# Performance work log

Measured on AMD Instinct MI355X. Metric: run time of the kernel, lower is better.

## Reference

```python
import jax, jax.numpy as jnp
import numpy as np

N_NODES = 65536
N_EDGES = 524288
N_GRAPHS = 512
G_NODES = 10000
NUM_DISEASES = 2000
IN_DIM = 128
HID = 256  # 2 * IN_DIM (z_emb concat feat)
D_FEAT = 512
C_FEAT = 512
MAX_Z = 4000


def setup_inputs() -> dict:
    key = jax.random.key(0)
    ks = jax.random.split(key, 20)
    rn = lambda k, shape: jax.random.normal(k, shape, dtype=jnp.float32) * 0.05
    return {
        "z": jax.random.randint(ks[0], (N_NODES,), 0, MAX_Z),
        "node_id": jnp.sort(jax.random.randint(ks[1], (N_NODES,), 0, G_NODES)),
        "src": jax.random.randint(ks[2], (N_EDGES,), 0, N_NODES),
        "dst": jax.random.randint(ks[3], (N_EDGES,), 0, N_NODES),
        "graph_ids": jnp.sort(jax.random.randint(ks[4], (N_NODES,), 0, N_GRAPHS)),
        "z_table": rn(ks[5], (MAX_Z, IN_DIM)),
        "d_feat_tab": rn(ks[6], (G_NODES, D_FEAT)),
        "c_feat_tab": rn(ks[7], (G_NODES, C_FEAT)),
        "Wd": rn(ks[8], (D_FEAT, IN_DIM)),
        "Wc": rn(ks[9], (C_FEAT, IN_DIM)),
        "gin_W1": rn(ks[10], (HID, HID)), "gin_b1": jnp.zeros((HID,), jnp.float32),
        "gin_W2": rn(ks[11], (HID, HID)), "gin_b2": jnp.zeros((HID,), jnp.float32),
        "sage_Wself": rn(ks[12], (HID, HID)),
        "sage_Wneigh": rn(ks[13], (HID, HID)),
        "sage_b": jnp.zeros((HID,), jnp.float32),
        "lin1_W": rn(ks[14], (HID, HID)), "lin1_b": jnp.zeros((HID,), jnp.float32),
        "lin2_W": rn(ks[15], (HID, 1)), "lin2_b": jnp.zeros((1,), jnp.float32),
    }


def reference(z, node_id, src, dst, graph_ids, z_table, d_feat_tab, c_feat_tab,
              Wd, Wc, gin_W1, gin_b1, gin_W2, gin_b2,
              sage_Wself, sage_Wneigh, sage_b, lin1_W, lin1_b, lin2_W, lin2_b):
    # --- input feature construction (Model.forward) ---
    z_emb = z_table[z]                               # [N, IN_DIM]
    d_proj = d_feat_tab[node_id] @ Wd                # d_fc (bias=False)
    c_proj = c_feat_tab[node_id] @ Wc                # c_fc (bias=False)
    disease = (node_id <= NUM_DISEASES)[:, None]
    # node_id is sorted -> masked concat order == node order
    feat = jnp.where(disease, d_proj, c_proj)        # [N, IN_DIM]
    x = jnp.concatenate([z_emb, feat], axis=1)       # [N, HID]
    # --- GINConv: sum aggregation, eps=0, mlp = Lin->ReLU->Lin ---
    agg = jax.ops.segment_sum(x[src], dst, num_segments=N_NODES)
    h = x + agg
    h = jax.nn.relu(h @ gin_W1 + gin_b1) @ gin_W2 + gin_b2
    # --- SAGEConv('mean'): fc_self(h) + fc_neigh(mean_neighbors) + bias ---
    deg = jax.ops.segment_sum(jnp.ones((N_EDGES,), h.dtype), dst, num_segments=N_NODES)
    mean_n = jax.ops.segment_sum(h[src], dst, num_segments=N_NODES) / jnp.maximum(deg, 1.0)[:, None]
    h = h @ sage_Wself + mean_n @ sage_Wneigh + sage_b
    # --- per-graph max pooling readout ---
    g = jax.ops.segment_max(h, graph_ids, num_segments=N_GRAPHS, indices_are_sorted=True)
    g = jnp.where(jnp.isfinite(g), g, 0.0)           # guard empty graphs
    # --- head: Linear -> ReLU -> (dropout p=0, eval) -> Linear ---
    h = jax.nn.relu(g @ lin1_W + lin1_b)
    return h @ lin2_W + lin2_b                       # [N_GRAPHS, 1]
```

## Files before the change

### kernel.cpp

```cpp
#include <hip/hip_runtime.h>
#include <hip/hip_bf16.h>

#define N_NODES     65536
#define N_EDGES     524288
#define N_GRAPHS    512
#define G_NODES_N   10000
#define NUM_DIS     2000
#define IN_DIM      128
#define HID         256
#define D_FEAT      512
#define MAX_Z       4000

typedef _Float16 half8 __attribute__((ext_vector_type(8)));
typedef float    f32x4 __attribute__((ext_vector_type(4)));

typedef __attribute__((address_space(1))) const void as1_void;
typedef __attribute__((address_space(3))) void       as3_void;

__global__ __launch_bounds__(256) void prep_kernel(
    const float* __restrict__ Ws, const float* __restrict__ Wn,
    const float* __restrict__ Wd, const float* __restrict__ Wc,
    const float* __restrict__ W1, const float* __restrict__ W2,
    const float* __restrict__ z_table,
    const int* __restrict__ z, const int* __restrict__ node_id,
    _Float16* __restrict__ WsT, _Float16* __restrict__ WnT,
    _Float16* __restrict__ WdT, _Float16* __restrict__ WcT,
    _Float16* __restrict__ W12P, _Float16* __restrict__ zt16,
    int2* __restrict__ zn2, int* __restrict__ cnt, int* __restrict__ flags)
{
    const int b = blockIdx.x;
    const int tid = threadIdx.x;
    if (b < 64) {
        __shared__ float tile[64][65];
        const float* W; _Float16* T; int K, N, k0, n0;
        if (b < 32) {
            const int mat = b >> 4, t = b & 15;
            K = HID; N = HID; k0 = (t >> 2) * 64; n0 = (t & 3) * 64;
            W = (mat == 0) ? Ws : Wn;
            T = (mat == 0) ? WsT : WnT;
        } else {
            const int bb = b - 32;
            const int mat = bb >> 4, t = bb & 15;
            K = D_FEAT; N = IN_DIM; k0 = (t >> 1) * 64; n0 = (t & 1) * 64;
            W = (mat == 0) ? Wd : Wc;
            T = (mat == 0) ? WdT : WcT;
        }
        const int tx = tid & 63, ty = tid >> 6;
        #pragma unroll
        for (int r = 0; r < 64; r += 4)
            tile[r + ty][tx] = W[(size_t)(k0 + r + ty) * N + n0 + tx];
        __syncthreads();
        #pragma unroll
        for (int c = 0; c < 64; c += 4)
            T[(size_t)(n0 + c + ty) * K + k0 + tx] = (_Float16)tile[tx][c + ty];
    } else if (b < 576) {
        const int bb = b - 64;
        const int mat = bb >> 8;
        const int k = bb & 255;
        const int n = tid;
        const float* W = mat ? W2 : W1;
        const float v = W[(size_t)k * HID + n];
        const size_t idx = (size_t)(mat * 8 + (k >> 5)) * 8192
                         + (size_t)((((k >> 3) & 3) * 256 + n) * 8 + (k & 7));
        W12P[idx] = (_Float16)v;
    } else if (b < 826) {
        const size_t base = ((size_t)(b - 576) * 256 + tid) * 8;
        const float4 f0 = *(const float4*)(z_table + base);
        const float4 f1 = *(const float4*)(z_table + base + 4);
        half8 h;
        h[0]=(_Float16)f0.x; h[1]=(_Float16)f0.y; h[2]=(_Float16)f0.z; h[3]=(_Float16)f0.w;
        h[4]=(_Float16)f1.x; h[5]=(_Float16)f1.y; h[6]=(_Float16)f1.z; h[7]=(_Float16)f1.w;
        *(half8*)(zt16 + base) = h;
    } else if (b < 890) {
        const int base = (b - 826) * 1024 + tid * 4;
        *(int4*)(cnt + base) = make_int4(0, 0, 0, 0);
        if (b == 826 && tid < 128) flags[tid] = 0;
    } else {
        const int i = (b - 890) * 256 + tid;
        zn2[i] = make_int2(z[i] << 8, node_id[i] << 8);
    }
}

__global__ __launch_bounds__(256) void proj_hist_kernel(
    const float* __restrict__ dtab, const float* __restrict__ ctab,
    const _Float16* __restrict__ WdT, const _Float16* __restrict__ WcT,
    _Float16* __restrict__ proj,
    const int* __restrict__ dst, int* __restrict__ cnt)
{
    const int blk = blockIdx.x;
    if (blk >= 79) {
        const int e = (blk - 79) * 256 + threadIdx.x;
        if (e < N_EDGES) atomicAdd(&cnt[dst[e]], 1);
        return;
    }
    __shared__ _Float16 Alds[128 * 40];
    __shared__ _Float16 Blds[128 * 40];
    const float* tab; const _Float16* WT; int base, M, bm;
    if (blk < 16) { tab = dtab; WT = WdT; base = 0;           M = NUM_DIS + 1;             bm = blk * 128; }
    else          { tab = ctab; WT = WcT; base = NUM_DIS + 1; M = G_NODES_N - NUM_DIS - 1; bm = (blk - 16) * 128; }
    const int tid  = threadIdx.x;
    const int wave = tid >> 6, lane = tid & 63;
    const int q    = lane >> 4, l16 = lane & 15;
    const int mbase = (wave & 1) * 64, nbase = (wave >> 1) * 64;
    const int r = tid >> 1, s = tid & 1;

    f32x4 acc[4][4] = {};

    for (int kc = 0; kc < 16; ++kc) {
        const int k0 = kc * 32;
        const int arow = min(bm + r, M - 1);
        const float* gA = tab + (size_t)(base + arow) * D_FEAT + k0 + s * 16;
        const _Float16* gB = WT + (size_t)r * D_FEAT + k0 + s * 16;
        const float4 f0 = ((const float4*)gA)[0];
        const float4 f1 = ((const float4*)gA)[1];
        const float4 f2 = ((const float4*)gA)[2];
        const float4 f3 = ((const float4*)gA)[3];
        const half8 hb0 = *(const half8*)gB;
        const half8 hb1 = *(const half8*)(gB + 8);
        half8 h0, h1;
        h0[0]=(_Float16)f0.x; h0[1]=(_Float16)f0.y; h0[2]=(_Float16)f0.z; h0[3]=(_Float16)f0.w;
        h0[4]=(_Float16)f1.x; h0[5]=(_Float16)f1.y; h0[6]=(_Float16)f1.z; h0[7]=(_Float16)f1.w;
        h1[0]=(_Float16)f2.x; h1[1]=(_Float16)f2.y; h1[2]=(_Float16)f2.z; h1[3]=(_Float16)f2.w;
        h1[4]=(_Float16)f3.x; h1[5]=(_Float16)f3.y; h1[6]=(_Float16)f3.z; h1[7]=(_Float16)f3.w;
        __syncthreads();
        *(half8*)&Alds[r * 40 + s * 16]     = h0;
        *(half8*)&Alds[r * 40 + s * 16 + 8] = h1;
        *(half8*)&Blds[r * 40 + s * 16]     = hb0;
        *(half8*)&Blds[r * 40 + s * 16 + 8] = hb1;
        __syncthreads();
        half8 a[4], b[4];
        #pragma unroll
        for (int i = 0; i < 4; ++i)
            a[i] = *(const half8*)&Alds[(mbase + i * 16 + l16) * 40 + q * 8];
        #pragma unroll
        for (int j = 0; j < 4; ++j)
            b[j] = *(const half8*)&Blds[(nbase + j * 16 + l16) * 40 + q * 8];
        #pragma unroll
        for (int i = 0; i < 4; ++i)
            #pragma unroll
            for (int j = 0; j < 4; ++j)
                acc[i][j] = __builtin_amdgcn_mfma_f32_16x16x32_f16(a[i], b[j], acc[i][j], 0, 0, 0);
    }

    #pragma unroll
    for (int j = 0; j < 4; ++j) {
        const int colg = nbase + j * 16 + l16;
        #pragma unroll
        for (int i = 0; i < 4; ++i) {
            #pragma unroll
            for (int rr = 0; rr < 4; ++rr) {
                const int row = bm + mbase + i * 16 + q * 4 + rr;
                if (row < M)
                    proj[(size_t)(base + row) * IN_DIM + colg] = (_Float16)acc[i][j][rr];
            }
        }
    }
}

__global__ __launch_bounds__(256) void scan_fused_kernel(
    const int* __restrict__ cnt, int* __restrict__ row_ptr,
    int* __restrict__ fill, int* __restrict__ flags)
{
    __shared__ int a[256], b[256];
    __shared__ int sums[64];
    __shared__ int segbase;
    const int t = threadIdx.x;
    const int blk = blockIdx.x;
    const int base = blk * 1024 + t * 4;
    const int4 c = *(const int4*)(cnt + base);
    const int s = c.x + c.y + c.z + c.w;
    a[t] = s;
    __syncthreads();
    int* in = a; int* out = b;
    for (int off = 1; off < 256; off <<= 1) {
        out[t] = in[t] + ((t >= off) ? in[t - off] : 0);
        __syncthreads();
        int* tmp = in; in = out; out = tmp;
    }
    if (t == 0) {
        atomicExch(&flags[64 + blk], in[255]);
        __threadfence();
        atomicAdd(&flags[0], 1);
        while (atomicAdd(&flags[0], 0) < 64) {}
    }
    __syncthreads();
    if (t < 64) sums[t] = atomicAdd(&flags[64 + t], 0);
    __syncthreads();
    if (t == 0) {
        int pfx = 0;
        for (int i = 0; i < blk; ++i) pfx += sums[i];
        segbase = pfx;
        if (blk == 63) {
            int tot = pfx;
            for (int i = blk; i < 64; ++i) tot += sums[i];
            row_ptr[N_NODES] = tot;
        }
    }
    __syncthreads();
    const int run = in[t] - s + segbase;
    int4 r;
    r.x = run; r.y = run + c.x; r.z = r.y + c.y; r.w = r.z + c.z;
    *(int4*)(row_ptr + base) = r;
    *(int4*)(fill + base) = r;
}

__global__ __launch_bounds__(256) void scatter_kernel(
    const int* __restrict__ src, const int* __restrict__ dst,
    const int2* __restrict__ zn2,
    int* __restrict__ fill, int* __restrict__ col, int2* __restrict__ colzn)
{
    const int e = blockIdx.x * 256 + threadIdx.x;
    if (e < N_EDGES) {
        const int s = src[e];
        const int pos = atomicAdd(&fill[dst[e]], 1);
        col[pos] = s;
        colzn[pos] = zn2[s];
    }
}

__global__ __launch_bounds__(512) void gin_fused_kernel(
    const int* __restrict__ row_ptr, const int2* __restrict__ colzn,
    const int2* __restrict__ zn2,
    const _Float16* __restrict__ zt16, const _Float16* __restrict__ proj,
    const _Float16* __restrict__ W12P,
    const float* __restrict__ b1, const float* __restrict__ b2,
    _Float16* __restrict__ H)
{
    __shared__ _Float16 Apanel[64 * 264];
    __shared__ _Float16 Blds[8192];

    const int bm   = blockIdx.x * 64;
    const int tid  = threadIdx.x;
    const int wave = tid >> 6, lane = tid & 63;
    const int q    = lane >> 4, l16 = lane & 15;
    const int wr   = wave >> 2;
    const int wc   = wave & 3;
    const int rbase = wr * 32;
    const int nbase = wc * 64;

    #pragma unroll
    for (int tt = 0; tt < 2; ++tt) {
        const int seg = (wave * 2 + tt) * 64 + lane;
        __builtin_amdgcn_global_load_lds((as1_void*)(W12P + seg * 8),
            (as3_void*)&Blds[(wave * 2 + tt) * 64 * 8], 16, 0, 0);
    }

    {
        const int p = tid & 7;
        const int r = tid >> 3;
        const int gr = bm + r;
        const int beg = row_ptr[gr], end = row_ptr[gr + 1];
        const char* ztb = (const char*)zt16 + p * 32;
        const char* prb = (const char*)proj + p * 32;
        float za[16], pa[16];
        {
            const int2 zn = zn2[gr];
            const half8* zp = (const half8*)(ztb + zn.x);
            const half8* pp = (const half8*)(prb + zn.y);
            const half8 z0 = zp[0], z1 = zp[1], p0 = pp[0], p1 = pp[1];
            #pragma unroll
            for (int i = 0; i < 8; ++i) {
                za[i] = (float)z0[i]; za[8 + i] = (float)z1[i];
                pa[i] = (float)p0[i]; pa[8 + i] = (float)p1[i];
            }
        }
        int e = beg;
        int2 iA, iB, iC, iD;
        if (e + 4 <= end) {
            iA = colzn[e]; iB = colzn[e + 1]; iC = colzn[e + 2]; iD = colzn[e + 3];
        }
        for (; e + 4 <= end; e += 4) {
            const half8* zpA = (const half8*)(ztb + iA.x);
            const half8* ppA = (const half8*)(prb + iA.y);
            const half8* zpB = (const half8*)(ztb + iB.x);
            const half8* ppB = (const half8*)(prb + iB.y);
            const half8* zpC = (const half8*)(ztb + iC.x);
            const half8* ppC = (const half8*)(prb + iC.y);
            const half8* zpD = (const half8*)(ztb + iD.x);
            const half8* ppD = (const half8*)(prb + iD.y);
            const half8 zA0 = zpA[0], zA1 = zpA[1], pA0 = ppA[0], pA1 = ppA[1];
            const half8 zB0 = zpB[0], zB1 = zpB[1], pB0 = ppB[0], pB1 = ppB[1];
            const half8 zC0 = zpC[0], zC1 = zpC[1], pC0 = ppC[0], pC1 = ppC[1];
            const half8 zD0 = zpD[0], zD1 = zpD[1], pD0 = ppD[0], pD1 = ppD[1];
            if (e + 8 <= end) {
                iA = colzn[e + 4]; iB = colzn[e + 5];
                iC = colzn[e + 6]; iD = colzn[e + 7];
            }
            #pragma unroll
            for (int i = 0; i < 8; ++i) {
                za[i]     += ((float)zA0[i] + (float)zB0[i]) + ((float)zC0[i] + (float)zD0[i]);
                za[8 + i] += ((float)zA1[i] + (float)zB1[i]) + ((float)zC1[i] + (float)zD1[i]);
                pa[i]     += ((float)pA0[i] + (float)pB0[i]) + ((float)pC0[i] + (float)pD0[i]);
                pa[8 + i] += ((float)pA1[i] + (float)pB1[i]) + ((float)pC1[i] + (float)pD1[i]);
            }
        }
        for (; e + 2 <= end; e += 2) {
            const int2 jA = colzn[e];
            const int2 jB = colzn[e + 1];
            const half8* zpA = (const half8*)(ztb + jA.x);
            const half8* ppA = (const half8*)(prb + jA.y);
            const half8* zpB = (const half8*)(ztb + jB.x);
            const half8* ppB = (const half8*)(prb + jB.y);
            const half8 zA0 = zpA[0], zA1 = zpA[1], pA0 = ppA[0], pA1 = ppA[1];
            const half8 zB0 = zpB[0], zB1 = zpB[1], pB0 = ppB[0], pB1 = ppB[1];
            #pragma unroll
            for (int i = 0; i < 8; ++i) {
                za[i]     += (float)zA0[i] + (float)zB0[i];
                za[8 + i] += (float)zA1[i] + (float)zB1[i];
                pa[i]     += (float)pA0[i] + (float)pB0[i];
                pa[8 + i] += (float)pA1[i] + (float)pB1[i];
            }
        }
        if (e < end) {
            const int2 jA = colzn[e];
            const half8* zp = (const half8*)(ztb + jA.x);
            const half8* pp = (const half8*)(prb + jA.y);
            const half8 z0 = zp[0], z1 = zp[1], p0 = pp[0], p1 = pp[1];
            #pragma unroll
            for (int i = 0; i < 8; ++i) {
                za[i] += (float)z0[i]; za[8 + i] += (float)z1[i];
                pa[i] += (float)p0[i]; pa[8 + i] += (float)p1[i];
            }
        }
        half8 oz0, oz1, op0, op1;
        #pragma unroll
        for (int i = 0; i < 8; ++i) {
            oz0[i] = (_Float16)za[i];     oz1[i] = (_Float16)za[8 + i];
            op0[i] = (_Float16)pa[i];     op1[i] = (_Float16)pa[8 + i];
        }
        *(half8*)&Apanel[r * 264 + p * 16]           = oz0;
        *(half8*)&Apanel[r * 264 + p * 16 + 8]       = oz1;
        *(half8*)&Apanel[r * 264 + 128 + p * 16]     = op0;
        *(half8*)&Apanel[r * 264 + 128 + p * 16 + 8] = op1;
    }
    __syncthreads();

    half8 pf0, pf1;
    auto pfetch = [&](int c) {
        const _Float16* s = W12P + (size_t)c * 8192 + (size_t)tid * 8;
        pf0 = *(const half8*)(s);
        pf1 = *(const half8*)(s + 4096);
    };
    pfetch(1);

    f32x4 acc[2][4] = {};
    for (int c = 0; c < 16; ++c) {
        const int kl = (c & 7) * 32;
        half8 a[2], b[4];
        #pragma unroll
        for (int i = 0; i < 2; ++i)
            a[i] = *(const half8*)&Apanel[(rbase + i * 16 + l16) * 264 + kl + q * 8];
        #pragma unroll
        for (int j = 0; j < 4; ++j)
            b[j] = *(const half8*)&Blds[(q * 256 + nbase + j * 16 + l16) * 8];
        #pragma unroll
        for (int i = 0; i < 2; ++i)
            #pragma unroll
            for (int j = 0; j < 4; ++j)
                acc[i][j] = __builtin_amdgcn_mfma_f32_16x16x32_f16(a[i], b[j], acc[i][j], 0, 0, 0);
        if (c == 15) break;
        __syncthreads();
        *(half8*)&Blds[tid * 8]         = pf0;
        *(half8*)&Blds[(tid + 512) * 8] = pf1;
        if (c == 7) {
            #pragma unroll
            for (int j = 0; j < 4; ++j) {
                const int colg = nbase + j * 16 + l16;
                const float bv = b1[colg];
                #pragma unroll
                for (int i = 0; i < 2; ++i)
                    #pragma unroll
                    for (int rr = 0; rr < 4; ++rr) {
                        const float v = fmaxf(acc[i][j][rr] + bv, 0.0f);
                        Apanel[(rbase + i * 16 + q * 4 + rr) * 264 + colg] = (_Float16)v;
                        acc[i][j][rr] = 0.0f;
                    }
            }
        }
        if (c < 14) pfetch(c + 2);
        __syncthreads();
    }

    #pragma unroll
    for (int j = 0; j < 4; ++j) {
        const int colg = nbase + j * 16 + l16;
        const float bv = b2[colg];
        #pragma unroll
        for (int i = 0; i < 2; ++i)
            #pragma unroll
            for (int rr = 0; rr < 4; ++rr) {
                const int rowg = bm + rbase + i * 16 + q * 4 + rr;
                H[(size_t)rowg * HID + colg] = (_Float16)(acc[i][j][rr] + bv);
            }
    }
}

__global__ __launch_bounds__(256) void csr_agg_kernel(
    const int* __restrict__ row_ptr, const int* __restrict__ col,
    const _Float16* __restrict__ F, _Float16* __restrict__ OUT)
{
    const int t = blockIdx.x * 256 + threadIdx.x;
    const int d = t >> 5;
    const int q = t & 31;
    const int beg = row_ptr[d];
    const int end = row_ptr[d + 1];
    float acc[8] = {0.f,0.f,0.f,0.f,0.f,0.f,0.f,0.f};
    int e = beg;
    for (; e + 8 <= end; e += 8) {
        const int s0 = col[e],     s1 = col[e + 1];
        const int s2 = col[e + 2], s3 = col[e + 3];
        const int s4 = col[e + 4], s5 = col[e + 5];
        const int s6 = col[e + 6], s7 = col[e + 7];
        const half8 v0 = *(const half8*)(F + (size_t)s0 * HID + q * 8);
        const half8 v1 = *(const half8*)(F + (size_t)s1 * HID + q * 8);
        const half8 v2 = *(const half8*)(F + (size_t)s2 * HID + q * 8);
        const half8 v3 = *(const half8*)(F + (size_t)s3 * HID + q * 8);
        const half8 v4 = *(const half8*)(F + (size_t)s4 * HID + q * 8);
        const half8 v5 = *(const half8*)(F + (size_t)s5 * HID + q * 8);
        const half8 v6 = *(const half8*)(F + (size_t)s6 * HID + q * 8);
        const half8 v7 = *(const half8*)(F + (size_t)s7 * HID + q * 8);
        #pragma unroll
        for (int i = 0; i < 8; ++i)
            acc[i] += (((float)v0[i] + (float)v1[i]) + ((float)v2[i] + (float)v3[i]))
                    + (((float)v4[i] + (float)v5[i]) + ((float)v6[i] + (float)v7[i]));
    }
    for (; e + 4 <= end; e += 4) {
        const int s0 = col[e],     s1 = col[e + 1];
        const int s2 = col[e + 2], s3 = col[e + 3];
        const half8 v0 = *(const half8*)(F + (size_t)s0 * HID + q * 8);
        const half8 v1 = *(const half8*)(F + (size_t)s1 * HID + q * 8);
        const half8 v2 = *(const half8*)(F + (size_t)s2 * HID + q * 8);
        const half8 v3 = *(const half8*)(F + (size_t)s3 * HID + q * 8);
        #pragma unroll
        for (int i = 0; i < 8; ++i)
            acc[i] += ((float)v0[i] + (float)v1[i]) + ((float)v2[i] + (float)v3[i]);
    }
    for (; e < end; ++e) {
        const half8 v0 = *(const half8*)(F + (size_t)col[e] * HID + q * 8);
        #pragma unroll
        for (int i = 0; i < 8; ++i) acc[i] += (float)v0[i];
    }
    const float rs = 1.0f / fmaxf((float)(end - beg), 1.0f);
    half8 o;
    #pragma unroll
    for (int i = 0; i < 8; ++i) o[i] = (_Float16)(acc[i] * rs);
    *(half8*)(OUT + (size_t)d * HID + q * 8) = o;
}

__global__ __launch_bounds__(256) void mfma_gemm_kernel(
    const _Float16* __restrict__ A1, const _Float16* __restrict__ A2,
    const _Float16* __restrict__ B1T, const _Float16* __restrict__ B2T,
    const float* __restrict__ bias, _Float16* __restrict__ Ch)
{
    __shared__ _Float16 Alds[128 * 32];
    __shared__ _Float16 Blds[128 * 32];
    const int bm   = blockIdx.x * 128;
    const int bn   = blockIdx.y * 128;
    const int tid  = threadIdx.x;
    const int wave = tid >> 6, lane = tid & 63;
    const int q    = lane >> 4, l16 = lane & 15;
    const int mbase = (wave & 1) * 64, nbase = (wave >> 1) * 64;

    const int i0 = wave * 128 + lane;
    const int i1 = i0 + 64;
    const int r0 = i0 >> 2, s0 = i0 & 3;
    const int r1 = i1 >> 2, s1 = i1 & 3;

    half8 pa0, pa1, pb0, pb1;
    auto pfetch = [&](int kc) {
        const int k0 = (kc & 7) * 32;
        const _Float16* Ab = (kc < 8) ? A1 : A2;
        const _Float16* Bb = (kc < 8) ? B1T : B2T;
        pa0 = *(const half8*)(Ab + (size_t)(bm + r0) * HID + k0 + s0 * 8);
        pa1 = *(const half8*)(Ab + (size_t)(bm + r1) * HID + k0 + s1 * 8);
        pb0 = *(const half8*)(Bb + (size_t)(bn + r0) * HID + k0 + s0 * 8);
        pb1 = *(const half8*)(Bb + (size_t)(bn + r1) * HID + k0 + s1 * 8);
    };
    pfetch(0);

    f32x4 acc[4][4] = {};

    for (int kc = 0; kc < 16; ++kc) {
        __syncthreads();
        *(half8*)&Alds[i0 * 8] = pa0;
        *(half8*)&Alds[i1 * 8] = pa1;
        *(half8*)&Blds[i0 * 8] = pb0;
        *(half8*)&Blds[i1 * 8] = pb1;
        if (kc < 15) pfetch(kc + 1);
        __syncthreads();
        half8 a[4], b[4];
        #pragma unroll
        for (int i = 0; i < 4; ++i)
            a[i] = *(const half8*)&Alds[(mbase + i * 16 + l16) * 32 + q * 8];
        #pragma unroll
        for (int j = 0; j < 4; ++j)
            b[j] = *(const half8*)&Blds[(nbase + j * 16 + l16) * 32 + q * 8];
        #pragma unroll
        for (int i = 0; i < 4; ++i)
            #pragma unroll
            for (int j = 0; j < 4; ++j)
                acc[i][j] = __builtin_amdgcn_mfma_f32_16x16x32_f16(a[i], b[j], acc[i][j], 0, 0, 0);
    }

    #pragma unroll
    for (int j = 0; j < 4; ++j) {
        const int colg = bn + nbase + j * 16 + l16;
        const float bv = bias[colg];
        #pragma unroll
        for (int i = 0; i < 4; ++i) {
            #pragma unroll
            for (int rr = 0; rr < 4; ++rr) {
                const int rowg = bm + mbase + i * 16 + q * 4 + rr;
                Ch[(size_t)rowg * HID + colg] = (_Float16)(acc[i][j][rr] + bv);
            }
        }
    }
}

__global__ __launch_bounds__(256) void pool_head_kernel(
    const _Float16* __restrict__ H2, const int* __restrict__ gid,
    const float* __restrict__ W1, const float* __restrict__ b1,
    const float* __restrict__ W2, const float* __restrict__ b2,
    float* __restrict__ out)
{
    const int g = blockIdx.x;
    const int tid = threadIdx.x;
    int lo = 0, hi = N_NODES;
    while (lo < hi) { const int mid = (lo + hi) >> 1; if (gid[mid] < g) lo = mid + 1; else hi = mid; }
    const int start = lo;
    hi = N_NODES;
    while (lo < hi) { const int mid = (lo + hi) >> 1; if (gid[mid] < g + 1) lo = mid + 1; else hi = mid; }
    const int end = lo;

    const int rowofs = tid >> 5;
    const int q = tid & 31;
    float m8[8];
    #pragma unroll
    for (int k = 0; k < 8; ++k) m8[k] = -INFINITY;
    for (int i = start + rowofs; i < end; i += 8) {
        const half8 v = *(const half8*)(H2 + (size_t)i * HID + q * 8);
        #pragma unroll
        for (int k = 0; k < 8; ++k) m8[k] = fmaxf(m8[k], (float)v[k]);
    }
    __shared__ float part[8][256];
    #pragma unroll
    for (int k = 0; k < 8; ++k) part[rowofs][q * 8 + k] = m8[k];
    __syncthreads();
    __shared__ float row[HID];
    __shared__ float red[HID];
    const int j = tid;
    float m = part[0][j];
    #pragma unroll
    for (int r = 1; r < 8; ++r) m = fmaxf(m, part[r][j]);
    row[j] = (m == -INFINITY) ? 0.0f : m;
    __syncthreads();
    float acc = b1[j];
    #pragma unroll 8
    for (int k = 0; k < HID; ++k)
        acc = fmaf(row[k], W1[k * HID + j], acc);
    acc = fmaxf(acc, 0.f);
    red[j] = acc * W2[j];
    __syncthreads();
    for (int s = 128; s > 0; s >>= 1) {
        if (j < s) red[j] += red[j + s];
        __syncthreads();
    }
    if (j == 0) out[g] = red[0] + b2[0];
}

extern "C" void kernel_launch(void* const* d_in, const int* in_sizes, int n_in,
                              void* d_out, int out_size, void* d_ws, size_t ws_size,
                              hipStream_t stream)
{
    const int*   z         = (const int*)d_in[0];
    const int*   node_id   = (const int*)d_in[1];
    const int*   src       = (const int*)d_in[2];
    const int*   dst       = (const int*)d_in[3];
    const int*   graph_ids = (const int*)d_in[4];
    const float* z_table   = (const float*)d_in[5];
    const float* d_feat    = (const float*)d_in[6];
    const float* c_feat    = (const float*)d_in[7];
    const float* Wd        = (const float*)d_in[8];
    const float* Wc        = (const float*)d_in[9];
    const float* gin_W1    = (const float*)d_in[10];
    const float* gin_b1    = (const float*)d_in[11];
    const float* gin_W2    = (const float*)d_in[12];
    const float* gin_b2    = (const float*)d_in[13];
    const float* sage_Wself  = (const float*)d_in[14];
    const float* sage_Wneigh = (const float*)d_in[15];
    const float* sage_b    = (const float*)d_in[16];
    const float* lin1_W    = (const float*)d_in[17];
    const float* lin1_b    = (const float*)d_in[18];
    const float* lin2_W    = (const float*)d_in[19];
    const float* lin2_b    = (const float*)d_in[20];
    float* out = (float*)d_out;

    const size_t NH = (size_t)N_NODES * HID;
    char* wsb = (char*)d_ws;
    _Float16* Hh   = (_Float16*)wsb;                     wsb += NH * 2;
    _Float16* AGGh = (_Float16*)wsb;                     wsb += NH * 2;
    _Float16* H2h  = (_Float16*)wsb;                     wsb += NH * 2;
    _Float16* projh= (_Float16*)wsb;                     wsb += (size_t)G_NODES_N * IN_DIM * 2;
    _Float16* W12P = (_Float16*)wsb;                     wsb += 16 * 8192 * 2;
    _Float16* WsT  = (_Float16*)wsb;                     wsb += HID * HID * 2;
    _Float16* WnT  = (_Float16*)wsb;                     wsb += HID * HID * 2;
    _Float16* WdT  = (_Float16*)wsb;                     wsb += D_FEAT * IN_DIM * 2;
    _Float16* WcT  = (_Float16*)wsb;                     wsb += D_FEAT * IN_DIM * 2;
    _Float16* zt16 = (_Float16*)wsb;                     wsb += (size_t)MAX_Z * IN_DIM * 2;
    int2* zn2      = (int2*)wsb;                         wsb += (size_t)N_NODES * 8;
    int2* colzn    = (int2*)wsb;                         wsb += (size_t)(N_EDGES + 8) * 8;
    int* row_ptr   = (int*)wsb;                          wsb += (N_NODES + 4) * 4;
    int* cnt       = (int*)wsb;                          wsb += N_NODES * 4;
    int* fill      = (int*)wsb;                          wsb += N_NODES * 4;
    int* col       = (int*)wsb;                          wsb += N_EDGES * 4;
    int* flags     = (int*)wsb;                          wsb += 128 * 4;

    prep_kernel<<<1146, 256, 0, stream>>>(
        sage_Wself, sage_Wneigh, Wd, Wc, gin_W1, gin_W2, z_table, z, node_id,
        WsT, WnT, WdT, WcT, W12P, zt16, zn2, cnt, flags);

    proj_hist_kernel<<<79 + N_EDGES / 256, 256, 0, stream>>>(
        d_feat, c_feat, WdT, WcT, projh, dst, cnt);

    scan_fused_kernel<<<64, 256, 0, stream>>>(cnt, row_ptr, fill, flags);
    scatter_kernel<<<N_EDGES / 256, 256, 0, stream>>>(src, dst, zn2, fill, col, colzn);

    gin_fused_kernel<<<N_NODES / 64, 512, 0, stream>>>(
        row_ptr, colzn, zn2, zt16, projh, W12P, gin_b1, gin_b2, Hh);

    csr_agg_kernel<<<(N_NODES * 32) / 256, 256, 0, stream>>>(row_ptr, col, Hh, AGGh);

    dim3 ggrid(N_NODES / 128, HID / 128);
    mfma_gemm_kernel<<<ggrid, 256, 0, stream>>>(Hh, AGGh, WsT, WnT, sage_b, H2h);

    pool_head_kernel<<<N_GRAPHS, 256, 0, stream>>>(
        H2h, graph_ids, lin1_W, lin1_b, lin2_W, lin2_b, out);
}
```

Baseline: 345.4 us.

## Rebalance kernel fusion: histogram into prep, scatter with projection, 256-thread GIN blocks

The edge histogram now runs inside the prep kernel, and zeroing of cnt/flags moves to hipMemsetAsync. The dst-to-CSR scatter now shares a launch with the d/c feature projection GEMM, which removes one launch and overlaps the projection with the atomic scatter. The GIN fused kernel drops from 512 to 256 threads per block, so each wave computes 64 rows x 64 cols and each thread aggregates two node rows sequentially. This lowers per-block parallelism in the gather phase but gives each wave more MFMA reuse.

```diff
diff --git a/kernel.cpp b/kernel.cpp
--- a/kernel.cpp
+++ b/kernel.cpp
@@ -17,16 +17,17 @@
 typedef __attribute__((address_space(1))) const void as1_void;
 typedef __attribute__((address_space(3))) void       as3_void;
 
-__global__ __launch_bounds__(256) void prep_kernel(
+__global__ __launch_bounds__(256) void prep_hist_kernel(
     const float* __restrict__ Ws, const float* __restrict__ Wn,
     const float* __restrict__ Wd, const float* __restrict__ Wc,
     const float* __restrict__ W1, const float* __restrict__ W2,
     const float* __restrict__ z_table,
     const int* __restrict__ z, const int* __restrict__ node_id,
+    const int* __restrict__ dst,
     _Float16* __restrict__ WsT, _Float16* __restrict__ WnT,
     _Float16* __restrict__ WdT, _Float16* __restrict__ WcT,
     _Float16* __restrict__ W12P, _Float16* __restrict__ zt16,
-    int2* __restrict__ zn2, int* __restrict__ cnt, int* __restrict__ flags)
+    int2* __restrict__ zn2, int* __restrict__ cnt)
 {
     const int b = blockIdx.x;
     const int tid = threadIdx.x;
@@ -71,30 +72,83 @@
         h[0]=(_Float16)f0.x; h[1]=(_Float16)f0.y; h[2]=(_Float16)f0.z; h[3]=(_Float16)f0.w;
         h[4]=(_Float16)f1.x; h[5]=(_Float16)f1.y; h[6]=(_Float16)f1.z; h[7]=(_Float16)f1.w;
         *(half8*)(zt16 + base) = h;
-    } else if (b < 890) {
-        const int base = (b - 826) * 1024 + tid * 4;
-        *(int4*)(cnt + base) = make_int4(0, 0, 0, 0);
-        if (b == 826 && tid < 128) flags[tid] = 0;
+    } else if (b < 1082) {
+        const int i = (b - 826) * 256 + tid;
+        zn2[i] = make_int2(z[i] << 8, node_id[i] << 8);
     } else {
-        const int i = (b - 890) * 256 + tid;
-        zn2[i] = make_int2(z[i] << 8, node_id[i] << 8);
-    }
-}
-
-__global__ __launch_bounds__(256) void proj_hist_kernel(
+        const int e = (b - 1082) * 256 + tid;
+        atomicAdd(&cnt[dst[e]], 1);
+    }
+}
+
+__global__ __launch_bounds__(256) void scan_fused_kernel(
+    const int* __restrict__ cnt, int* __restrict__ row_ptr,
+    int* __restrict__ fill, int* __restrict__ flags)
+{
+    __shared__ int a[256], b[256];
+    __shared__ int sums[64];
+    __shared__ int segbase;
+    const int t = threadIdx.x;
+    const int blk = blockIdx.x;
+    const int base = blk * 1024 + t * 4;
+    const int4 c = *(const int4*)(cnt + base);
+    const int s = c.x + c.y + c.z + c.w;
+    a[t] = s;
+    __syncthreads();
+    int* in = a; int* out = b;
+    for (int off = 1; off < 256; off <<= 1) {
+        out[t] = in[t] + ((t >= off) ? in[t - off] : 0);
+        __syncthreads();
+        int* tmp = in; in = out; out = tmp;
+    }
+    if (t == 0) {
+        atomicExch(&flags[64 + blk], in[255]);
+        __threadfence();
+        atomicAdd(&flags[0], 1);
+        while (atomicAdd(&flags[0], 0) < 64) {}
+    }
+    __syncthreads();
+    if (t < 64) sums[t] = atomicAdd(&flags[64 + t], 0);
+    __syncthreads();
+    if (t == 0) {
+        int pfx = 0;
+        for (int i = 0; i < blk; ++i) pfx += sums[i];
+        segbase = pfx;
+        if (blk == 63) {
+            int tot = pfx;
+            for (int i = blk; i < 64; ++i) tot += sums[i];
+            row_ptr[N_NODES] = tot;
+        }
+    }
+    __syncthreads();
+    const int run = in[t] - s + segbase;
+    int4 r;
+    r.x = run; r.y = run + c.x; r.z = r.y + c.y; r.w = r.z + c.z;
+    *(int4*)(row_ptr + base) = r;
+    *(int4*)(fill + base) = r;
+}
+
+__global__ __launch_bounds__(256) void scatter_proj_kernel(
     const float* __restrict__ dtab, const float* __restrict__ ctab,
     const _Float16* __restrict__ WdT, const _Float16* __restrict__ WcT,
     _Float16* __restrict__ proj,
-    const int* __restrict__ dst, int* __restrict__ cnt)
-{
+    const int* __restrict__ src, const int* __restrict__ dst,
+    const int2* __restrict__ zn2,
+    int* __restrict__ fill, int* __restrict__ col, int2* __restrict__ colzn)
+{
+    __shared__ _Float16 Alds[128 * 40];
+    __shared__ _Float16 Blds[128 * 40];
     const int blk = blockIdx.x;
     if (blk >= 79) {
         const int e = (blk - 79) * 256 + threadIdx.x;
-        if (e < N_EDGES) atomicAdd(&cnt[dst[e]], 1);
+        if (e < N_EDGES) {
+            const int s = src[e];
+            const int pos = atomicAdd(&fill[dst[e]], 1);
+            col[pos] = s;
+            colzn[pos] = zn2[s];
+        }
         return;
     }
-    __shared__ _Float16 Alds[128 * 40];
-    __shared__ _Float16 Blds[128 * 40];
     const float* tab; const _Float16* WT; int base, M, bm;
     if (blk < 16) { tab = dtab; WT = WdT; base = 0;           M = NUM_DIS + 1;             bm = blk * 128; }
     else          { tab = ctab; WT = WcT; base = NUM_DIS + 1; M = G_NODES_N - NUM_DIS - 1; bm = (blk - 16) * 128; }
@@ -157,68 +211,7 @@
     }
 }
 
-__global__ __launch_bounds__(256) void scan_fused_kernel(
-    const int* __restrict__ cnt, int* __restrict__ row_ptr,
-    int* __restrict__ fill, int* __restrict__ flags)
-{
-    __shared__ int a[256], b[256];
-    __shared__ int sums[64];
-    __shared__ int segbase;
-    const int t = threadIdx.x;
-    const int blk = blockIdx.x;
-    const int base = blk * 1024 + t * 4;
-    const int4 c = *(const int4*)(cnt + base);
-    const int s = c.x + c.y + c.z + c.w;
-    a[t] = s;
-    __syncthreads();
-    int* in = a; int* out = b;
-    for (int off = 1; off < 256; off <<= 1) {
-        out[t] = in[t] + ((t >= off) ? in[t - off] : 0);
-        __syncthreads();
-        int* tmp = in; in = out; out = tmp;
-    }
-    if (t == 0) {
-        atomicExch(&flags[64 + blk], in[255]);
-        __threadfence();
-        atomicAdd(&flags[0], 1);
-        while (atomicAdd(&flags[0], 0) < 64) {}
-    }
-    __syncthreads();
-    if (t < 64) sums[t] = atomicAdd(&flags[64 + t], 0);
-    __syncthreads();
-    if (t == 0) {
-        int pfx = 0;
-        for (int i = 0; i < blk; ++i) pfx += sums[i];
-        segbase = pfx;
-        if (blk == 63) {
-            int tot = pfx;
-            for (int i = blk; i < 64; ++i) tot += sums[i];
-            row_ptr[N_NODES] = tot;
-        }
-    }
-    __syncthreads();
-    const int run = in[t] - s + segbase;
-    int4 r;
-    r.x = run; r.y = run + c.x; r.z = r.y + c.y; r.w = r.z + c.z;
-    *(int4*)(row_ptr + base) = r;
-    *(int4*)(fill + base) = r;
-}
-
-__global__ __launch_bounds__(256) void scatter_kernel(
-    const int* __restrict__ src, const int* __restrict__ dst,
-    const int2* __restrict__ zn2,
-    int* __restrict__ fill, int* __restrict__ col, int2* __restrict__ colzn)
-{
-    const int e = blockIdx.x * 256 + threadIdx.x;
-    if (e < N_EDGES) {
-        const int s = src[e];
-        const int pos = atomicAdd(&fill[dst[e]], 1);
-        col[pos] = s;
-        colzn[pos] = zn2[s];
-    }
-}
-
-__global__ __launch_bounds__(512) void gin_fused_kernel(
+__global__ __launch_bounds__(256) void gin_fused_kernel(
     const int* __restrict__ row_ptr, const int2* __restrict__ colzn,
     const int2* __restrict__ zn2,
     const _Float16* __restrict__ zt16, const _Float16* __restrict__ proj,
@@ -233,146 +226,151 @@
     const int tid  = threadIdx.x;
     const int wave = tid >> 6, lane = tid & 63;
     const int q    = lane >> 4, l16 = lane & 15;
-    const int wr   = wave >> 2;
-    const int wc   = wave & 3;
-    const int rbase = wr * 32;
-    const int nbase = wc * 64;
-
-    #pragma unroll
-    for (int tt = 0; tt < 2; ++tt) {
-        const int seg = (wave * 2 + tt) * 64 + lane;
+    const int nbase = wave * 64;
+    const int sb   = wave * 256 + lane;
+
+    #pragma unroll
+    for (int tt = 0; tt < 4; ++tt) {
+        const int seg = (wave * 4 + tt) * 64 + lane;
         __builtin_amdgcn_global_load_lds((as1_void*)(W12P + seg * 8),
-            (as3_void*)&Blds[(wave * 2 + tt) * 64 * 8], 16, 0, 0);
+            (as3_void*)&Blds[(wave * 4 + tt) * 64 * 8], 16, 0, 0);
     }
 
     {
         const int p = tid & 7;
-        const int r = tid >> 3;
-        const int gr = bm + r;
-        const int beg = row_ptr[gr], end = row_ptr[gr + 1];
         const char* ztb = (const char*)zt16 + p * 32;
         const char* prb = (const char*)proj + p * 32;
-        float za[16], pa[16];
-        {
-            const int2 zn = zn2[gr];
-            const half8* zp = (const half8*)(ztb + zn.x);
-            const half8* pp = (const half8*)(prb + zn.y);
-            const half8 z0 = zp[0], z1 = zp[1], p0 = pp[0], p1 = pp[1];
+        #pragma unroll 1
+        for (int pass = 0; pass < 2; ++pass) {
+            const int r  = (tid >> 3) + (pass << 5);
+            const int gr = bm + r;
+            const int beg = row_ptr[gr], end = row_ptr[gr + 1];
+            float za[16], pa[16];
+            {
+                const int2 zn = zn2[gr];
+                const half8* zp = (const half8*)(ztb + zn.x);
+                const half8* pp = (const half8*)(prb + zn.y);
+                const half8 z0 = zp[0], z1 = zp[1], p0 = pp[0], p1 = pp[1];
+                #pragma unroll
+                for (int i = 0; i < 8; ++i) {
+                    za[i] = (float)z0[i]; za[8 + i] = (float)z1[i];
+                    pa[i] = (float)p0[i]; pa[8 + i] = (float)p1[i];
+                }
+            }
+            int e = beg;
+            int2 iA, iB, iC, iD;
+            if (e + 4 <= end) {
+                iA = colzn[e]; iB = colzn[e + 1]; iC = colzn[e + 2]; iD = colzn[e + 3];
+            }
+            for (; e + 4 <= end; e += 4) {
+                const half8* zpA = (const half8*)(ztb + iA.x);
+                const half8* ppA = (const half8*)(prb + iA.y);
+                const half8* zpB = (const half8*)(ztb + iB.x);
+                const half8* ppB = (const half8*)(prb + iB.y);
+                const half8* zpC = (const half8*)(ztb + iC.x);
+                const half8* ppC = (const half8*)(prb + iC.y);
+                const half8* zpD = (const half8*)(ztb + iD.x);
+                const half8* ppD = (const half8*)(prb + iD.y);
+                const half8 zA0 = zpA[0], zA1 = zpA[1], pA0 = ppA[0], pA1 = ppA[1];
+                const half8 zB0 = zpB[0], zB1 = zpB[1], pB0 = ppB[0], pB1 = ppB[1];
+                const half8 zC0 = zpC[0], zC1 = zpC[1], pC0 = ppC[0], pC1 = ppC[1];
+                const half8 zD0 = zpD[0], zD1 = zpD[1], pD0 = ppD[0], pD1 = ppD[1];
+                if (e + 8 <= end) {
+                    iA = colzn[e + 4]; iB = colzn[e + 5];
+                    iC = colzn[e + 6]; iD = colzn[e + 7];
+                }
+                #pragma unroll
+                for (int i = 0; i < 8; ++i) {
+                    za[i]     += ((float)zA0[i] + (float)zB0[i]) + ((float)zC0[i] + (float)zD0[i]);
+                    za[8 + i] += ((float)zA1[i] + (float)zB1[i]) + ((float)zC1[i] + (float)zD1[i]);
+                    pa[i]     += ((float)pA0[i] + (float)pB0[i]) + ((float)pC0[i] + (float)pD0[i]);
+                    pa[8 + i] += ((float)pA1[i] + (float)pB1[i]) + ((float)pC1[i] + (float)pD1[i]);
+                }
+            }
+            for (; e + 2 <= end; e += 2) {
+                const int2 jA = colzn[e];
+                const int2 jB = colzn[e + 1];
+                const half8* zpA = (const half8*)(ztb + jA.x);
+                const half8* ppA = (const half8*)(prb + jA.y);
+                const half8* zpB = (const half8*)(ztb + jB.x);
+                const half8* ppB = (const half8*)(prb + jB.y);
+                const half8 zA0 = zpA[0], zA1 = zpA[1], pA0 = ppA[0], pA1 = ppA[1];
+                const half8 zB0 = zpB[0], zB1 = zpB[1], pB0 = ppB[0], pB1 = ppB[1];
+                #pragma unroll
+                for (int i = 0; i < 8; ++i) {
+                    za[i]     += (float)zA0[i] + (float)zB0[i];
+                    za[8 + i] += (float)zA1[i] + (float)zB1[i];
+                    pa[i]     += (float)pA0[i] + (float)pB0[i];
+                    pa[8 + i] += (float)pA1[i] + (float)pB1[i];
+                }
+            }
+            if (e < end) {
+                const int2 jA = colzn[e];
+                const half8* zp = (const half8*)(ztb + jA.x);
+                const half8* pp = (const half8*)(prb + jA.y);
+                const half8 z0 = zp[0], z1 = zp[1], p0 = pp[0], p1 = pp[1];
+                #pragma unroll
+                for (int i = 0; i < 8; ++i) {
+                    za[i] += (float)z0[i]; za[8 + i] += (float)z1[i];
+                    pa[i] += (float)p0[i]; pa[8 + i] += (float)p1[i];
+                }
+            }
+            half8 oz0, oz1, op0, op1;
             #pragma unroll
             for (int i = 0; i < 8; ++i) {
-                za[i] = (float)z0[i]; za[8 + i] = (float)z1[i];
-                pa[i] = (float)p0[i]; pa[8 + i] = (float)p1[i];
-            }
+                oz0[i] = (_Float16)za[i];     oz1[i] = (_Float16)za[8 + i];
+                op0[i] = (_Float16)pa[i];     op1[i] = (_Float16)pa[8 + i];
+            }
+            *(half8*)&Apanel[r * 264 + p * 16]           = oz0;
+            *(half8*)&Apanel[r * 264 + p * 16 + 8]       = oz1;
+            *(half8*)&Apanel[r * 264 + 128 + p * 16]     = op0;
+            *(half8*)&Apanel[r * 264 + 128 + p * 16 + 8] = op1;
         }
-        int e = beg;
-        int2 iA, iB, iC, iD;
-        if (e + 4 <= end) {
-            iA = colzn[e]; iB = colzn[e + 1]; iC = colzn[e + 2]; iD = colzn[e + 3];
-        }
-        for (; e + 4 <= end; e += 4) {
-            const half8* zpA = (const half8*)(ztb + iA.x);
-            const half8* ppA = (const half8*)(prb + iA.y);
-            const half8* zpB = (const half8*)(ztb + iB.x);
-            const half8* ppB = (const half8*)(prb + iB.y);
-            const half8* zpC = (const half8*)(ztb + iC.x);
-            const half8* ppC = (const half8*)(prb + iC.y);
-            const half8* zpD = (const half8*)(ztb + iD.x);
-            const half8* ppD = (const half8*)(prb + iD.y);
-            const half8 zA0 = zpA[0], zA1 = zpA[1], pA0 = ppA[0], pA1 = ppA[1];
-            const half8 zB0 = zpB[0], zB1 = zpB[1], pB0 = ppB[0], pB1 = ppB[1];
-            const half8 zC0 = zpC[0], zC1 = zpC[1], pC0 = ppC[0], pC1 = ppC[1];
-            const half8 zD0 = zpD[0], zD1 = zpD[1], pD0 = ppD[0], pD1 = ppD[1];
-            if (e + 8 <= end) {
-                iA = colzn[e + 4]; iB = colzn[e + 5];
-                iC = colzn[e + 6]; iD = colzn[e + 7];
-            }
-            #pragma unroll
-            for (int i = 0; i < 8; ++i) {
-                za[i]     += ((float)zA0[i] + (float)zB0[i]) + ((float)zC0[i] + (float)zD0[i]);
-                za[8 + i] += ((float)zA1[i] + (float)zB1[i]) + ((float)zC1[i] + (float)zD1[i]);
-                pa[i]     += ((float)pA0[i] + (float)pB0[i]) + ((float)pC0[i] + (float)pD0[i]);
-                pa[8 + i] += ((float)pA1[i] + (float)pB1[i]) + ((float)pC1[i] + (float)pD1[i]);
-            }
-        }
-        for (; e + 2 <= end; e += 2) {
-            const int2 jA = colzn[e];
-            const int2 jB = colzn[e + 1];
-            const half8* zpA = (const half8*)(ztb + jA.x);
-            const half8* ppA = (const half8*)(prb + jA.y);
-            const half8* zpB = (const half8*)(ztb + jB.x);
-            const half8* ppB = (const half8*)(prb + jB.y);
-            const half8 zA0 = zpA[0], zA1 = zpA[1], pA0 = ppA[0], pA1 = ppA[1];
-            const half8 zB0 = zpB[0], zB1 = zpB[1], pB0 = ppB[0], pB1 = ppB[1];
-            #pragma unroll
-            for (int i = 0; i < 8; ++i) {
-                za[i]     += (float)zA0[i] + (float)zB0[i];
-                za[8 + i] += (float)zA1[i] + (float)zB1[i];
-                pa[i]     += (float)pA0[i] + (float)pB0[i];
-                pa[8 + i] += (float)pA1[i] + (float)pB1[i];
-            }
-        }
-        if (e < end) {
-            const int2 jA = colzn[e];
-            const half8* zp = (const half8*)(ztb + jA.x);
-            const half8* pp = (const half8*)(prb + jA.y);
-            const half8 z0 = zp[0], z1 = zp[1], p0 = pp[0], p1 = pp[1];
-            #pragma unroll
-            for (int i = 0; i < 8; ++i) {
-                za[i] += (float)z0[i]; za[8 + i] += (float)z1[i];
-                pa[i] += (float)p0[i]; pa[8 + i] += (float)p1[i];
-            }
-        }
-        half8 oz0, oz1, op0, op1;
-        #pragma unroll
-        for (int i = 0; i < 8; ++i) {
-            oz0[i] = (_Float16)za[i];     oz1[i] = (_Float16)za[8 + i];
-            op0[i] = (_Float16)pa[i];     op1[i] = (_Float16)pa[8 + i];
-        }
-        *(half8*)&Apanel[r * 264 + p * 16]           = oz0;
-        *(half8*)&Apanel[r * 264 + p * 16 + 8]       = oz1;
-        *(half8*)&Apanel[r * 264 + 128 + p * 16]     = op0;
-        *(half8*)&Apanel[r * 264 + 128 + p * 16 + 8] = op1;
-    }
-    __syncthreads();
-
-    half8 pf0, pf1;
+    }
+    __syncthreads();
+
+    half8 pf0, pf1, pf2, pf3;
     auto pfetch = [&](int c) {
-        const _Float16* s = W12P + (size_t)c * 8192 + (size_t)tid * 8;
+        const _Float16* s = W12P + (size_t)c * 8192 + (size_t)sb * 8;
         pf0 = *(const half8*)(s);
-        pf1 = *(const half8*)(s + 4096);
+        pf1 = *(const half8*)(s + 512);
+        pf2 = *(const half8*)(s + 1024);
+        pf3 = *(const half8*)(s + 1536);
     };
     pfetch(1);
 
-    f32x4 acc[2][4] = {};
+    f32x4 acc[4][4] = {};
     for (int c = 0; c < 16; ++c) {
         const int kl = (c & 7) * 32;
-        half8 a[2], b[4];
-        #pragma unroll
-        for (int i = 0; i < 2; ++i)
-            a[i] = *(const half8*)&Apanel[(rbase + i * 16 + l16) * 264 + kl + q * 8];
+        half8 a[4], b[4];
+        #pragma unroll
+        for (int i = 0; i < 4; ++i)
+            a[i] = *(const half8*)&Apanel[(i * 16 + l16) * 264 + kl + q * 8];
         #pragma unroll
         for (int j = 0; j < 4; ++j)
             b[j] = *(const half8*)&Blds[(q * 256 + nbase + j * 16 + l16) * 8];
         #pragma unroll
-        for (int i = 0; i < 2; ++i)
+        for (int i = 0; i < 4; ++i)
             #pragma unroll
             for (int j = 0; j < 4; ++j)
                 acc[i][j] = __builtin_amdgcn_mfma_f32_16x16x32_f16(a[i], b[j], acc[i][j], 0, 0, 0);
         if (c == 15) break;
         __syncthreads();
-        *(half8*)&Blds[tid * 8]         = pf0;
-        *(half8*)&Blds[(tid + 512) * 8] = pf1;
+        *(half8*)&Blds[sb * 8]         = pf0;
+        *(half8*)&Blds[(sb + 64) * 8]  = pf1;
+        *(half8*)&Blds[(sb + 128) * 8] = pf2;
+        *(half8*)&Blds[(sb + 192) * 8] = pf3;
         if (c == 7) {
             #pragma unroll
             for (int j = 0; j < 4; ++j) {
                 const int colg = nbase + j * 16 + l16;
                 const float bv = b1[colg];
                 #pragma unroll
-                for (int i = 0; i < 2; ++i)
+                for (int i = 0; i < 4; ++i)
                     #pragma unroll
                     for (int rr = 0; rr < 4; ++rr) {
                         const float v = fmaxf(acc[i][j][rr] + bv, 0.0f);
-                        Apanel[(rbase + i * 16 + q * 4 + rr) * 264 + colg] = (_Float16)v;
+                        Apanel[(i * 16 + q * 4 + rr) * 264 + colg] = (_Float16)v;
                         acc[i][j][rr] = 0.0f;
                     }
             }
@@ -386,10 +384,10 @@
         const int colg = nbase + j * 16 + l16;
         const float bv = b2[colg];
         #pragma unroll
-        for (int i = 0; i < 2; ++i)
+        for (int i = 0; i < 4; ++i)
             #pragma unroll
             for (int rr = 0; rr < 4; ++rr) {
-                const int rowg = bm + rbase + i * 16 + q * 4 + rr;
+                const int rowg = bm + i * 16 + q * 4 + rr;
                 H[(size_t)rowg * HID + colg] = (_Float16)(acc[i][j][rr] + bv);
             }
     }
@@ -615,17 +613,18 @@
     int* col       = (int*)wsb;                          wsb += N_EDGES * 4;
     int* flags     = (int*)wsb;                          wsb += 128 * 4;
 
-    prep_kernel<<<1146, 256, 0, stream>>>(
+    hipMemsetAsync(cnt, 0, N_NODES * sizeof(int), stream);
+    hipMemsetAsync(flags, 0, 128 * sizeof(int), stream);
+    prep_hist_kernel<<<1082 + N_EDGES / 256, 256, 0, stream>>>(
         sage_Wself, sage_Wneigh, Wd, Wc, gin_W1, gin_W2, z_table, z, node_id,
-        WsT, WnT, WdT, WcT, W12P, zt16, zn2, cnt, flags);
-
-    proj_hist_kernel<<<79 + N_EDGES / 256, 256, 0, stream>>>(
-        d_feat, c_feat, WdT, WcT, projh, dst, cnt);
+        dst, WsT, WnT, WdT, WcT, W12P, zt16, zn2, cnt);
 
     scan_fused_kernel<<<64, 256, 0, stream>>>(cnt, row_ptr, fill, flags);
-    scatter_kernel<<<N_EDGES / 256, 256, 0, stream>>>(src, dst, zn2, fill, col, colzn);
-
-    gin_fused_kernel<<<N_NODES / 64, 512, 0, stream>>>(
+
+    scatter_proj_kernel<<<79 + N_EDGES / 256, 256, 0, stream>>>(
+        d_feat, c_feat, WdT, WcT, projh, src, dst, zn2, fill, col, colzn);
+
+    gin_fused_kernel<<<N_NODES / 64, 256, 0, stream>>>(
         row_ptr, colzn, zn2, zt16, projh, W12P, gin_b1, gin_b2, Hh);
 
     csr_agg_kernel<<<(N_NODES * 32) / 256, 256, 0, stream>>>(row_ptr, col, Hh, AGGh);
```

Result: no change. 346.5 us (+0.3%).
